# Kernel tuning notes

Measured on AMD Instinct MI355X. Metric: run time of the kernel, lower is better.

The kernel has to match this reference:

```python
import jax, jax.numpy as jnp
import numpy as np

ALPHA = 0.2  # LeakyReLU negative slope
NEG_INF = -1e9


def setup_inputs() -> dict:
    key = jax.random.key(0)
    k1, k2, k3, k4 = jax.random.split(key, 4)
    B, N, IN, OUT = 8, 2048, 512, 32
    graph_input = jax.random.normal(k1, (B, N, IN), dtype=jnp.float32)
    adj = jax.random.randint(k2, (B, N, N), 0, 2, dtype=jnp.int32)
    W_fc = jax.random.normal(k3, (OUT, IN), dtype=jnp.float32) * (1.0 / np.sqrt(IN))
    W_attn = jax.random.normal(k4, (1, 2 * OUT), dtype=jnp.float32) * (1.0 / np.sqrt(2 * OUT))
    return {"graph_input": graph_input, "adj": adj, "W_fc": W_fc, "W_attn": W_attn}


def reference(graph_input, adj, W_fc, W_attn):
    # h: [B, N, 32]
    h = jnp.einsum('bni,oi->bno', graph_input, W_fc)
    out_dim = W_fc.shape[0]
    # attn_fc(cat(h_i, h_j)) is separable: a1.h_i + a2.h_j
    a1 = W_attn[0, :out_dim]   # [32]
    a2 = W_attn[0, out_dim:]   # [32]
    f1 = jnp.einsum('bno,o->bn', h, a1)  # [B, N]
    f2 = jnp.einsum('bno,o->bn', h, a2)  # [B, N]
    scores = jax.nn.leaky_relu(f1[:, :, None] + f2[:, None, :], negative_slope=ALPHA)  # [B,N,N]
    scores = jnp.where(adj == 0, NEG_INF, scores)
    attn = jax.nn.softmax(scores, axis=2)
    # NOTE: original multiplies attention with graph_input (not h)
    h_prime = jnp.einsum('bnm,bmi->bni', attn, graph_input)  # [B, N, IN]
    return jax.nn.elu(h_prime)  # concat=True path
```

## Files before the change

kernel.cpp:

```cpp
#include <hip/hip_runtime.h>
#include <hip/hip_bf16.h>

#define BATCH 8
#define NN    2048
#define FIN   512
#define FOUT  32
#define GALPHA 0.2f
#define RT    32
#define NIT   32

typedef float  f32x4  __attribute__((ext_vector_type(4)));
typedef __bf16 bf16x8 __attribute__((ext_vector_type(8)));
typedef unsigned short u16;
typedef u16 u16x8 __attribute__((ext_vector_type(8)));

static __device__ __forceinline__ u16 f2bf(float f) {
    __hip_bfloat16 h = __float2bfloat16(f);
    union { __hip_bfloat16 h; u16 u; } c; c.h = h; return c.u;
}
static __device__ __forceinline__ float bf2f(u16 u) {
    union { u16 u; __hip_bfloat16 h; } c; c.u = u; return __bfloat162float(c.h);
}

__global__ void k_w12(const float* __restrict__ Wfc,
                      const float* __restrict__ Wat,
                      float* __restrict__ w1, float* __restrict__ w2) {
    int i = threadIdx.x;
    float s1 = 0.f, s2 = 0.f;
    #pragma unroll
    for (int o = 0; o < FOUT; o++) {
        float wv = Wfc[o * FIN + i];
        s1 += wv * Wat[o];
        s2 += wv * Wat[FOUT + o];
    }
    w1[i] = s1; w2[i] = s2;
}

__global__ void k_xtf(const float* __restrict__ x,
                      const float* __restrict__ w1, const float* __restrict__ w2,
                      __hip_bfloat16* __restrict__ xt,
                      float* __restrict__ f1, float* __restrict__ f2) {
    int bx = blockIdx.x;
    int it = bx & 7, mt = (bx >> 3) & 31, b = bx >> 8;
    int m0 = mt * 64, i0 = it * 64;
    __shared__ u16 tile[64][72];
    int tt = threadIdx.x;
    int mm = tt >> 3;
    int ic = (tt & 7) * 8;
    const float* xb = x + ((size_t)b * NN + m0) * FIN + i0;
    const f32x4* w1p = (const f32x4*)(w1 + i0 + ic);
    const f32x4* w2p = (const f32x4*)(w2 + i0 + ic);
    f32x4 wA = w1p[0], wB = w1p[1], wC = w2p[0], wD = w2p[1];
    float p1[2], p2[2];
    #pragma unroll
    for (int h = 0; h < 2; h++) {
        int m = mm + h * 32;
        const f32x4* src = (const f32x4*)(xb + (size_t)m * FIN + ic);
        f32x4 v0 = src[0], v1 = src[1];
        u16x8 pk;
        float s1 = 0.f, s2 = 0.f;
        #pragma unroll
        for (int j = 0; j < 4; j++) {
            pk[j] = f2bf(v0[j]); pk[4 + j] = f2bf(v1[j]);
            s1 += v0[j] * wA[j] + v1[j] * wB[j];
            s2 += v0[j] * wC[j] + v1[j] * wD[j];
        }
        p1[h] = s1; p2[h] = s2;
        *(u16x8*)&tile[m][ic] = pk;
    }
    #pragma unroll
    for (int off = 1; off < 8; off <<= 1) {
        p1[0] += __shfl_xor(p1[0], off); p1[1] += __shfl_xor(p1[1], off);
        p2[0] += __shfl_xor(p2[0], off); p2[1] += __shfl_xor(p2[1], off);
    }
    if ((tt & 7) == 0) {
        size_t r0 = (size_t)b * NN + m0 + mm;
        atomicAdd(&f1[r0], p1[0]);      atomicAdd(&f1[r0 + 32], p1[1]);
        atomicAdd(&f2[r0], p2[0]);      atomicAdd(&f2[r0 + 32], p2[1]);
    }
    __syncthreads();
    __hip_bfloat16* xtb = xt + ((size_t)b * FIN + i0) * NN + m0;
    int mc = (tt & 7) * 8;
    #pragma unroll
    for (int h = 0; h < 2; h++) {
        int ii = (tt >> 3) + h * 32;
        u16x8 v;
        #pragma unroll
        for (int j = 0; j < 8; j++) v[j] = tile[mc + j][ii];
        *(u16x8*)(xtb + (size_t)ii * NN + mc) = v;
    }
}

__global__ __launch_bounds__(512, 4) void k_main(
    const int* __restrict__ adj, const __hip_bfloat16* __restrict__ xt,
    const float* __restrict__ f1, const float* __restrict__ f2,
    float* __restrict__ out)
{
    const int bx = blockIdx.x;
    const int b = bx & 7, rt = bx >> 3;
    const int n0 = rt * RT;
    const int tid = threadIdx.x;
    const int lane = tid & 63, wv = tid >> 6;
    const int quad = lane >> 4, l15 = lane & 15;

    __shared__ u16 At[2][RT * 64];
    __shared__ float rs[RT];

    const int grow = tid >> 4;
    const int gch  = (tid & 15) * 4;
    const int wofs = grow * 64 + (gch ^ (8 * (grow & 7)));
    const int*   adjp = adj + ((size_t)b * NN + (n0 + grow)) * NN + gch;
    const float* f2p  = f2 + b * NN + gch;
    const float  f1v  = f1[b * NN + n0 + grow];
    float rpart = 0.f;

    const __hip_bfloat16* xtp = xt + ((size_t)(b * FIN) + wv * 64 + l15) * NN + quad * 8;

    f32x4 acc[2][4];
    #pragma unroll
    for (int s = 0; s < 2; s++)
        #pragma unroll
        for (int c = 0; c < 4; c++)
            acc[s][c] = (f32x4){0.f, 0.f, 0.f, 0.f};

    auto gen = [&](int buf, int4 av, float4 fv) {
        const int*   ai = (const int*)&av;
        const float* fi = (const float*)&fv;
        ushort4 pk;
        u16* pp = (u16*)&pk;
        #pragma unroll
        for (int j = 0; j < 4; j++) {
            float s  = f1v + fi[j];
            float ls = fmaxf(s, GALPHA * s);
            float ev = (ai[j] != 0) ? __expf(ls) : 0.f;
            u16 hb = f2bf(ev);
            rpart += bf2f(hb);
            pp[j] = hb;
        }
        *(ushort4*)&At[buf][wofs] = pk;
    };

    int4   a0 = *(const int4*)adjp;
    float4 g0 = *(const float4*)f2p;
    int4   aring[2];
    float4 fring[2];
    gen(0, a0, g0);
    aring[1] = *(const int4*)(adjp + 64);
    fring[1] = *(const float4*)(f2p + 64);
    aring[0] = *(const int4*)(adjp + 128);
    fring[0] = *(const float4*)(f2p + 128);
    __syncthreads();

    #pragma unroll 2
    for (int t = 0; t < NIT; t++) {
        const int cur = t & 1;
        const __hip_bfloat16* xk = xtp + t * 64;
        bf16x8 B0[4], B1[4];
        #pragma unroll
        for (int c = 0; c < 4; c++) {
            B0[c] = *(const bf16x8*)(xk + (size_t)(c * 16) * NN);
            B1[c] = *(const bf16x8*)(xk + 32 + (size_t)(c * 16) * NN);
        }
        #pragma unroll
        for (int s = 0; s < 2; s++) {
            const int rsw = 8 * ((s * 16 + l15) & 7);
            bf16x8 Af0 = *(const bf16x8*)&At[cur][(s * 16 + l15) * 64 + ((quad * 8) ^ rsw)];
            #pragma unroll
            for (int c = 0; c < 4; c++)
                acc[s][c] = __builtin_amdgcn_mfma_f32_16x16x32_bf16(Af0, B0[c], acc[s][c], 0, 0, 0);
        }
        #pragma unroll
        for (int s = 0; s < 2; s++) {
            const int rsw = 8 * ((s * 16 + l15) & 7);
            bf16x8 Af1 = *(const bf16x8*)&At[cur][(s * 16 + l15) * 64 + ((32 + quad * 8) ^ rsw)];
            #pragma unroll
            for (int c = 0; c < 4; c++)
                acc[s][c] = __builtin_amdgcn_mfma_f32_16x16x32_bf16(Af1, B1[c], acc[s][c], 0, 0, 0);
        }
        if (t < NIT - 1) {
            gen(1 - cur, aring[(t + 1) & 1], fring[(t + 1) & 1]);
            if (t < NIT - 3) {
                aring[(t + 1) & 1] = *(const int4*)(adjp + (size_t)(t + 3) * 64);
                fring[(t + 1) & 1] = *(const float4*)(f2p + (size_t)(t + 3) * 64);
            }
        }
        asm volatile("s_waitcnt lgkmcnt(0)\ns_barrier" ::: "memory");
    }

    #pragma unroll
    for (int off = 1; off < 16; off <<= 1) rpart += __shfl_xor(rpart, off);
    if ((tid & 15) == 0) rs[grow] = 1.0f / rpart;
    __syncthreads();

    #pragma unroll
    for (int s = 0; s < 2; s++) {
        #pragma unroll
        for (int r = 0; r < 4; r++) {
            const int row = s * 16 + quad * 4 + r;
            const float inv = rs[row];
            float* op = out + ((size_t)b * NN + (n0 + row)) * FIN + wv * 64 + l15;
            #pragma unroll
            for (int c = 0; c < 4; c++) {
                float v = acc[s][c][r] * inv;
                v = v > 0.f ? v : (__expf(v) - 1.f);
                op[c * 16] = v;
            }
        }
    }
}

extern "C" void kernel_launch(void* const* d_in, const int* in_sizes, int n_in,
                              void* d_out, int out_size, void* d_ws, size_t ws_size,
                              hipStream_t stream) {
    const float* x   = (const float*)d_in[0];
    const int*   adj = (const int*)d_in[1];
    const float* Wfc = (const float*)d_in[2];
    const float* Wat = (const float*)d_in[3];
    float* out = (float*)d_out;

    float* w1 = (float*)d_ws;
    float* w2 = w1 + 512;
    float* f1 = w2 + 512;
    float* f2 = f1 + BATCH * NN;
    __hip_bfloat16* xt = (__hip_bfloat16*)(f2 + BATCH * NN);

    hipMemsetAsync(f1, 0, (size_t)2 * BATCH * NN * sizeof(float), stream);
    hipLaunchKernelGGL(k_w12, dim3(1),    dim3(512), 0, stream, Wfc, Wat, w1, w2);
    hipLaunchKernelGGL(k_xtf, dim3(2048), dim3(256), 0, stream, x, w1, w2, xt, f1, f2);
    hipLaunchKernelGGL(k_main, dim3(512), dim3(512), 0, stream, adj, xt, f1, f2, out);
}
```

Baseline: 341.0 us.

## Pack adjacency into bitmask and retile main kernel to 128 rows by 256 cols

Adds a pre-pass that compresses the int32 adjacency matrix into a per-row bitmask. The main kernel is retiled so each block covers 128 rows and a 256-wide slice of the output features, for 256 blocks instead of 512. Each wave now reuses its B fragments across 8 row subtiles, and the next step's B loads are prefetched into registers. The goal is more reuse of xt per MFMA and less adjacency traffic inside the main loop. The cost is an extra full pass over adj, with the softmax numerators recomputed twice (once per feature half), more registers, and fewer blocks.

```diff
diff --git a/kernel.cpp b/kernel.cpp
--- a/kernel.cpp
+++ b/kernel.cpp
@@ -6,7 +6,7 @@
 #define FIN   512
 #define FOUT  32
 #define GALPHA 0.2f
-#define RT    32
+#define NROW  128
 #define NIT   32
 
 typedef float  f32x4  __attribute__((ext_vector_type(4)));
@@ -91,116 +91,145 @@
     }
 }
 
-__global__ __launch_bounds__(512, 4) void k_main(
-    const int* __restrict__ adj, const __hip_bfloat16* __restrict__ xt,
+__global__ void k_pack(const int* __restrict__ adj, unsigned int* __restrict__ bits) {
+    int row  = blockIdx.x * 4 + (threadIdx.x >> 6);
+    int lane = threadIdx.x & 63;
+    const int* p = adj + (size_t)row * NN + lane * 32;
+    unsigned int bv = 0;
+    #pragma unroll
+    for (int j = 0; j < 8; j++) {
+        int4 v = *(const int4*)(p + j * 4);
+        bv |= (v.x != 0 ? 1u : 0u) << (j * 4 + 0);
+        bv |= (v.y != 0 ? 1u : 0u) << (j * 4 + 1);
+        bv |= (v.z != 0 ? 1u : 0u) << (j * 4 + 2);
+        bv |= (v.w != 0 ? 1u : 0u) << (j * 4 + 3);
+    }
+    bits[(size_t)row * 64 + lane] = bv;
+}
+
+__global__ __launch_bounds__(512, 2) void k_main(
+    const unsigned int* __restrict__ bits, const __hip_bfloat16* __restrict__ xt,
     const float* __restrict__ f1, const float* __restrict__ f2,
     float* __restrict__ out)
 {
     const int bx = blockIdx.x;
-    const int b = bx & 7, rt = bx >> 3;
-    const int n0 = rt * RT;
+    const int b = bx & 7, rt = (bx >> 3) & 15, it = bx >> 7;
+    const int n0 = rt * NROW;
+    const int i0 = it * 256;
     const int tid = threadIdx.x;
     const int lane = tid & 63, wv = tid >> 6;
     const int quad = lane >> 4, l15 = lane & 15;
 
-    __shared__ u16 At[2][RT * 64];
-    __shared__ float rs[RT];
-
-    const int grow = tid >> 4;
-    const int gch  = (tid & 15) * 4;
-    const int wofs = grow * 64 + (gch ^ (8 * (grow & 7)));
-    const int*   adjp = adj + ((size_t)b * NN + (n0 + grow)) * NN + gch;
-    const float* f2p  = f2 + b * NN + gch;
-    const float  f1v  = f1[b * NN + n0 + grow];
+    __shared__ u16 At[2][NROW * 64];
+    __shared__ float rs[NROW];
+
+    const int grow = tid >> 2;
+    const int q4   = tid & 3;
+    const unsigned short* bp = (const unsigned short*)bits
+                               + ((size_t)(b * NN) + n0 + grow) * 128 + q4;
+    const float* f2p = f2 + b * NN + q4 * 16;
+    const float  f1v = f1[b * NN + n0 + grow];
+    const int swz = grow & 7;
+    u16* wp0 = &At[0][grow * 64 + (((q4 * 2) ^ swz) * 8)];
+    u16* wp1 = &At[0][grow * 64 + (((q4 * 2 + 1) ^ swz) * 8)];
     float rpart = 0.f;
 
-    const __hip_bfloat16* xtp = xt + ((size_t)(b * FIN) + wv * 64 + l15) * NN + quad * 8;
-
-    f32x4 acc[2][4];
-    #pragma unroll
-    for (int s = 0; s < 2; s++)
-        #pragma unroll
-        for (int c = 0; c < 4; c++)
-            acc[s][c] = (f32x4){0.f, 0.f, 0.f, 0.f};
-
-    auto gen = [&](int buf, int4 av, float4 fv) {
-        const int*   ai = (const int*)&av;
-        const float* fi = (const float*)&fv;
-        ushort4 pk;
-        u16* pp = (u16*)&pk;
-        #pragma unroll
-        for (int j = 0; j < 4; j++) {
-            float s  = f1v + fi[j];
+    const __hip_bfloat16* xtp = xt + ((size_t)(b * FIN) + i0 + wv * 32 + l15) * NN + quad * 8;
+
+    f32x4 acc[8][2];
+    #pragma unroll
+    for (int s = 0; s < 8; s++) { acc[s][0] = (f32x4){0,0,0,0}; acc[s][1] = (f32x4){0,0,0,0}; }
+
+    auto gen = [&](int buf, unsigned int bv, const f32x4* fr) {
+        u16x8 pk0, pk1;
+        #pragma unroll
+        for (int e = 0; e < 16; e++) {
+            float s  = f1v + fr[e >> 2][e & 3];
             float ls = fmaxf(s, GALPHA * s);
-            float ev = (ai[j] != 0) ? __expf(ls) : 0.f;
+            float ev = ((bv >> e) & 1u) ? __expf(ls) : 0.f;
             u16 hb = f2bf(ev);
             rpart += bf2f(hb);
-            pp[j] = hb;
-        }
-        *(ushort4*)&At[buf][wofs] = pk;
+            if (e < 8) pk0[e] = hb; else pk1[e - 8] = hb;
+        }
+        *(u16x8*)(wp0 + buf * (NROW * 64)) = pk0;
+        *(u16x8*)(wp1 + buf * (NROW * 64)) = pk1;
     };
 
-    int4   a0 = *(const int4*)adjp;
-    float4 g0 = *(const float4*)f2p;
-    int4   aring[2];
-    float4 fring[2];
-    gen(0, a0, g0);
-    aring[1] = *(const int4*)(adjp + 64);
-    fring[1] = *(const float4*)(f2p + 64);
-    aring[0] = *(const int4*)(adjp + 128);
-    fring[0] = *(const float4*)(f2p + 128);
+    {
+        unsigned int b0 = bp[0];
+        f32x4 g0[4];
+        #pragma unroll
+        for (int j = 0; j < 4; j++) g0[j] = *(const f32x4*)(f2p + j * 4);
+        gen(0, b0, g0);
+    }
+    unsigned int brng[2];
+    f32x4 frng[2][4];
+    brng[1] = bp[4];
+    #pragma unroll
+    for (int j = 0; j < 4; j++) frng[1][j] = *(const f32x4*)(f2p + 64 + j * 4);
+    brng[0] = bp[8];
+    #pragma unroll
+    for (int j = 0; j < 4; j++) frng[0][j] = *(const f32x4*)(f2p + 128 + j * 4);
+
+    bf16x8 Bc[2][2], Bn[2][2];
+    #pragma unroll
+    for (int ks = 0; ks < 2; ks++)
+        #pragma unroll
+        for (int c = 0; c < 2; c++)
+            Bc[ks][c] = *(const bf16x8*)(xtp + ks * 32 + (size_t)(c * 16) * NN);
     __syncthreads();
 
     #pragma unroll 2
     for (int t = 0; t < NIT; t++) {
         const int cur = t & 1;
-        const __hip_bfloat16* xk = xtp + t * 64;
-        bf16x8 B0[4], B1[4];
-        #pragma unroll
-        for (int c = 0; c < 4; c++) {
-            B0[c] = *(const bf16x8*)(xk + (size_t)(c * 16) * NN);
-            B1[c] = *(const bf16x8*)(xk + 32 + (size_t)(c * 16) * NN);
-        }
-        #pragma unroll
-        for (int s = 0; s < 2; s++) {
-            const int rsw = 8 * ((s * 16 + l15) & 7);
-            bf16x8 Af0 = *(const bf16x8*)&At[cur][(s * 16 + l15) * 64 + ((quad * 8) ^ rsw)];
+        if (t < NIT - 1) {
+            const __hip_bfloat16* xk = xtp + (t + 1) * 64;
             #pragma unroll
-            for (int c = 0; c < 4; c++)
-                acc[s][c] = __builtin_amdgcn_mfma_f32_16x16x32_bf16(Af0, B0[c], acc[s][c], 0, 0, 0);
-        }
-        #pragma unroll
-        for (int s = 0; s < 2; s++) {
-            const int rsw = 8 * ((s * 16 + l15) & 7);
-            bf16x8 Af1 = *(const bf16x8*)&At[cur][(s * 16 + l15) * 64 + ((32 + quad * 8) ^ rsw)];
+            for (int ks = 0; ks < 2; ks++)
+                #pragma unroll
+                for (int c = 0; c < 2; c++)
+                    Bn[ks][c] = *(const bf16x8*)(xk + ks * 32 + (size_t)(c * 16) * NN);
+        }
+        #pragma unroll
+        for (int ks = 0; ks < 2; ks++) {
             #pragma unroll
-            for (int c = 0; c < 4; c++)
-                acc[s][c] = __builtin_amdgcn_mfma_f32_16x16x32_bf16(Af1, B1[c], acc[s][c], 0, 0, 0);
+            for (int s = 0; s < 8; s++) {
+                const int row = s * 16 + l15;
+                bf16x8 Af = *(const bf16x8*)&At[cur][row * 64 + (((ks * 4 + quad) ^ (row & 7)) * 8)];
+                acc[s][0] = __builtin_amdgcn_mfma_f32_16x16x32_bf16(Af, Bc[ks][0], acc[s][0], 0, 0, 0);
+                acc[s][1] = __builtin_amdgcn_mfma_f32_16x16x32_bf16(Af, Bc[ks][1], acc[s][1], 0, 0, 0);
+            }
         }
         if (t < NIT - 1) {
-            gen(1 - cur, aring[(t + 1) & 1], fring[(t + 1) & 1]);
-            if (t < NIT - 3) {
-                aring[(t + 1) & 1] = *(const int4*)(adjp + (size_t)(t + 3) * 64);
-                fring[(t + 1) & 1] = *(const float4*)(f2p + (size_t)(t + 3) * 64);
+            gen(1 - cur, brng[(t + 1) & 1], frng[(t + 1) & 1]);
+            if (t < NIT - 2) {
+                brng[t & 1] = bp[(t + 2) * 4];
+                #pragma unroll
+                for (int j = 0; j < 4; j++)
+                    frng[t & 1][j] = *(const f32x4*)(f2p + (t + 2) * 64 + j * 4);
             }
         }
         asm volatile("s_waitcnt lgkmcnt(0)\ns_barrier" ::: "memory");
-    }
-
-    #pragma unroll
-    for (int off = 1; off < 16; off <<= 1) rpart += __shfl_xor(rpart, off);
-    if ((tid & 15) == 0) rs[grow] = 1.0f / rpart;
+        #pragma unroll
+        for (int ks = 0; ks < 2; ks++) {
+            Bc[ks][0] = Bn[ks][0]; Bc[ks][1] = Bn[ks][1];
+        }
+    }
+
+    rpart += __shfl_xor(rpart, 1);
+    rpart += __shfl_xor(rpart, 2);
+    if (q4 == 0) rs[grow] = 1.0f / rpart;
     __syncthreads();
 
     #pragma unroll
-    for (int s = 0; s < 2; s++) {
+    for (int s = 0; s < 8; s++) {
         #pragma unroll
         for (int r = 0; r < 4; r++) {
             const int row = s * 16 + quad * 4 + r;
             const float inv = rs[row];
-            float* op = out + ((size_t)b * NN + (n0 + row)) * FIN + wv * 64 + l15;
+            float* op = out + ((size_t)b * NN + (n0 + row)) * FIN + i0 + wv * 32 + l15;
             #pragma unroll
-            for (int c = 0; c < 4; c++) {
+            for (int c = 0; c < 2; c++) {
                 float v = acc[s][c][r] * inv;
                 v = v > 0.f ? v : (__expf(v) - 1.f);
                 op[c * 16] = v;
@@ -222,10 +251,12 @@
     float* w2 = w1 + 512;
     float* f1 = w2 + 512;
     float* f2 = f1 + BATCH * NN;
-    __hip_bfloat16* xt = (__hip_bfloat16*)(f2 + BATCH * NN);
+    unsigned int* bits = (unsigned int*)(f2 + BATCH * NN);
+    __hip_bfloat16* xt = (__hip_bfloat16*)(bits + (size_t)BATCH * NN * 64);
 
     hipMemsetAsync(f1, 0, (size_t)2 * BATCH * NN * sizeof(float), stream);
-    hipLaunchKernelGGL(k_w12, dim3(1),    dim3(512), 0, stream, Wfc, Wat, w1, w2);
-    hipLaunchKernelGGL(k_xtf, dim3(2048), dim3(256), 0, stream, x, w1, w2, xt, f1, f2);
-    hipLaunchKernelGGL(k_main, dim3(512), dim3(512), 0, stream, adj, xt, f1, f2, out);
-}
+    hipLaunchKernelGGL(k_w12,  dim3(1),    dim3(512), 0, stream, Wfc, Wat, w1, w2);
+    hipLaunchKernelGGL(k_xtf,  dim3(2048), dim3(256), 0, stream, x, w1, w2, xt, f1, f2);
+    hipLaunchKernelGGL(k_pack, dim3(4096), dim3(256), 0, stream, adj, bits);
+    hipLaunchKernelGGL(k_main, dim3(256),  dim3(512), 0, stream, bits, xt, f1, f2, out);
+}
```

Result: faster. 285.9 us (-16.2%).
